# Optimization experiments

Hardware: AMD Instinct MI355X
Metric: run time of the kernel (lower is better)

Reference implementation:

```python
import jax, jax.numpy as jnp
import numpy as np

B, N, OUTERDIM, DIM, N_CLASSES = 2, 6000, 1024, 512, 2
HEADS, DIM_HEAD, INNER = 8, 64, 512
LANDMARKS, PINV_ITERS, KPAD = 256, 6, 16  # residual conv kernel 33 -> pad 16
SCALE = DIM_HEAD ** -0.5


def layer_norm(x, g, b, eps=1e-5):
    mu = x.mean(-1, keepdims=True)
    var = jnp.var(x, axis=-1, keepdims=True)
    return (x - mu) * jax.lax.rsqrt(var + eps) * g + b


def moore_penrose_pinv(x, iters=PINV_ITERS):
    # x: [b, h, m, m]
    abs_x = jnp.abs(x)
    col = abs_x.sum(-1)
    row = abs_x.sum(-2)
    z = jnp.swapaxes(x, -1, -2) / (jnp.max(col) * jnp.max(row))
    I = jnp.eye(x.shape[-1], dtype=x.dtype)
    for _ in range(iters):
        xz = x @ z
        z = 0.25 * z @ (13 * I - xz @ (15 * I - xz @ (7 * I - xz)))
    return z


def nystrom_attention(x, w_qkv, w_out, b_out, conv_w):
    b, n, _ = x.shape
    pad = (-n) % LANDMARKS
    xp = jnp.pad(x, ((0, 0), (pad, 0), (0, 0)))  # pad at FRONT, as in lucidrains impl
    npad = n + pad
    qkv = xp @ w_qkv.T  # [b, npad, 3*inner]
    q, k, v = [t.reshape(b, npad, HEADS, DIM_HEAD).transpose(0, 2, 1, 3)
               for t in jnp.split(qkv, 3, axis=-1)]
    q = q * SCALE
    l = npad // LANDMARKS  # tokens per landmark
    q_l = q.reshape(b, HEADS, LANDMARKS, l, DIM_HEAD).sum(3) / l
    k_l = k.reshape(b, HEADS, LANDMARKS, l, DIM_HEAD).sum(3) / l
    attn1 = jax.nn.softmax(jnp.einsum('bhid,bhjd->bhij', q, k_l), axis=-1)   # [b,h,npad,m]
    attn2 = jax.nn.softmax(jnp.einsum('bhid,bhjd->bhij', q_l, k_l), axis=-1)  # [b,h,m,m]
    attn3 = jax.nn.softmax(jnp.einsum('bhid,bhjd->bhij', q_l, k), axis=-1)    # [b,h,m,npad]
    out = (attn1 @ moore_penrose_pinv(attn2)) @ (attn3 @ v)  # [b,h,npad,d]
    # depthwise residual conv over sequence dim (per head), kernel (33,1)
    out = out + jax.lax.conv_general_dilated(
        v, conv_w, window_strides=(1, 1), padding=((KPAD, KPAD), (0, 0)),
        dimension_numbers=('NCHW', 'OIHW', 'NCHW'), feature_group_count=HEADS)
    out = out.transpose(0, 2, 1, 3).reshape(b, npad, INNER)
    out = out @ w_out.T + b_out
    return out[:, -n:]


def setup_inputs() -> dict:
    key = jax.random.key(0)
    ks = jax.random.split(key, 12)
    w = lambda k, shape: 0.02 * jax.random.normal(k, shape, dtype=jnp.float32)
    inp = {
        'data': jax.random.normal(ks[0], (B, N, OUTERDIM), dtype=jnp.float32),
        'w1': w(ks[1], (DIM, OUTERDIM)), 'b1': jnp.zeros((DIM,), jnp.float32),
        'cls_token': jax.random.normal(ks[2], (1, 1, DIM), dtype=jnp.float32),
        'ln1_g': jnp.ones((DIM,), jnp.float32), 'ln1_b': jnp.zeros((DIM,), jnp.float32),
        'qkv1_w': w(ks[3], (3 * INNER, DIM)),
        'out1_w': w(ks[4], (DIM, INNER)), 'out1_b': jnp.zeros((DIM,), jnp.float32),
        'conv1_w': w(ks[5], (HEADS, 1, 33, 1)),
        'ln2_g': jnp.ones((DIM,), jnp.float32), 'ln2_b': jnp.zeros((DIM,), jnp.float32),
        'qkv2_w': w(ks[6], (3 * INNER, DIM)),
        'out2_w': w(ks[7], (DIM, INNER)), 'out2_b': jnp.zeros((DIM,), jnp.float32),
        'conv2_w': w(ks[8], (HEADS, 1, 33, 1)),
        'lnf_g': jnp.ones((DIM,), jnp.float32), 'lnf_b': jnp.zeros((DIM,), jnp.float32),
        'w2': w(ks[9], (N_CLASSES, DIM)), 'b2': jnp.zeros((N_CLASSES,), jnp.float32),
    }
    return inp


def reference(data, w1, b1, cls_token, ln1_g, ln1_b, qkv1_w, out1_w, out1_b, conv1_w,
              ln2_g, ln2_b, qkv2_w, out2_w, out2_b, conv2_w, lnf_g, lnf_b, w2, b2):
    h = jax.nn.relu(data @ w1.T + b1)  # [B, N, DIM]
    H = h.shape[1]
    side = int(np.ceil(np.sqrt(H)))
    add = side * side - H
    h = jnp.concatenate([h, h[:, :add]], axis=1)  # square padding: 6084
    cls = jnp.broadcast_to(cls_token, (h.shape[0], 1, h.shape[2]))
    h = jnp.concatenate([cls, h], axis=1)  # +CLS: 6085
    h = h + nystrom_attention(layer_norm(h, ln1_g, ln1_b), qkv1_w, out1_w, out1_b, conv1_w)
    h = h + nystrom_attention(layer_norm(h, ln2_g, ln2_b), qkv2_w, out2_w, out2_b, conv2_w)
    h = layer_norm(h, lnf_g, lnf_b)[:, 0]
    logits = h @ w2.T + b2
    return logits
```

## Files before the change

### kernel.cpp

```cpp
#include <hip/hip_runtime.h>
#include <cstdint>
#include <cstddef>

namespace {

constexpr int DIMC  = 512;
constexpr int SEQ   = 6085;
constexpr int NPAD  = 6144;
constexpr int PADF  = 59;
constexpr int LMK   = 256;
constexpr int BHN   = 16;
constexpr int KSPL  = 16;
constexpr int MPADR = 6016;

typedef __attribute__((ext_vector_type(8))) short bf8_t;
typedef __attribute__((ext_vector_type(4))) float f4_t;

#define MFMA(a, b, c) __builtin_amdgcn_mfma_f32_16x16x32_bf16(a, b, c, 0, 0, 0)

#define SWZB(r, cu) (((((r) << 6) + ((cu) << 1))) ^ (((r) & 7) << 4))

#define GLDS16(gp, lp) __builtin_amdgcn_global_load_lds( \
    (const __attribute__((address_space(1))) void*)(gp), \
    (__attribute__((address_space(3))) void*)(lp), 16, 0, 0)

__device__ __forceinline__ ushort f2bf(float f) {
    union { float f; uint32_t u; } c{f};
    uint32_t u = c.u;
    return (ushort)((u + 0x7FFFu + ((u >> 16) & 1u)) >> 16);
}
__device__ __forceinline__ float bf2f(ushort u) {
    union { uint32_t u; float f; } c{(uint32_t)u << 16};
    return c.f;
}

__device__ __forceinline__ float waveSum(float v) {
#pragma unroll
    for (int o = 32; o > 0; o >>= 1) v += __shfl_xor(v, o, 64);
    return v;
}
__device__ __forceinline__ float waveMax(float v) {
#pragma unroll
    for (int o = 32; o > 0; o >>= 1) v = fmaxf(v, __shfl_xor(v, o, 64));
    return v;
}
__device__ __forceinline__ float blockSum256(float v, float* sm) {
    v = waveSum(v);
    __syncthreads();
    if ((threadIdx.x & 63) == 0) sm[threadIdx.x >> 6] = v;
    __syncthreads();
    return sm[0] + sm[1] + sm[2] + sm[3];
}
__device__ __forceinline__ float blockMax256(float v, float* sm) {
    v = waveMax(v);
    __syncthreads();
    if ((threadIdx.x & 63) == 0) sm[threadIdx.x >> 6] = v;
    __syncthreads();
    return fmaxf(fmaxf(sm[0], sm[1]), fmaxf(sm[2], sm[3]));
}
__device__ __forceinline__ float grpMax(float v) {
    v = fmaxf(v, __shfl_xor(v, 1, 64));
    v = fmaxf(v, __shfl_xor(v, 2, 64));
    v = fmaxf(v, __shfl_xor(v, 4, 64));
    v = fmaxf(v, __shfl_xor(v, 8, 64));
    return v;
}
__device__ __forceinline__ float grpSum(float v) {
    v += __shfl_xor(v, 1, 64);
    v += __shfl_xor(v, 2, 64);
    v += __shfl_xor(v, 4, 64);
    v += __shfl_xor(v, 8, 64);
    return v;
}

template<int EPI>
__global__ __launch_bounds__(256)
void gemm_bt(const ushort* __restrict__ A, const ushort* __restrict__ B,
             void* __restrict__ Cv, int M, int N, int K,
             int lda, int ldb, int ldc,
             long long sA, long long sB, long long sC,
             const float* __restrict__ bias, int relu,
             ushort* __restrict__ qp, ushort* __restrict__ kp, ushort* __restrict__ vp)
{
    __shared__ __align__(16) char As_s[128 * 128];
    __shared__ __align__(16) char Bs_s[128 * 128];
    const int z = blockIdx.z;
    const ushort* Ab = A + (size_t)z * sA;
    const ushort* Bb = B + (size_t)z * sB;
    const int row0 = blockIdx.y * 128, col0 = blockIdx.x * 128;
    const int tid = threadIdx.x, wid = tid >> 6, lane = tid & 63;
    const int wr = wid >> 1, wc = wid & 1, lr = lane & 15, kg = lane >> 4;
    const int srow = lane >> 3, sq = lane & 7;
    f4_t acc[4][4] = {};
    for (int k0 = 0; k0 < K; k0 += 64) {
        __syncthreads();
#pragma unroll
        for (int i = 0; i < 4; ++i) {
            int r = wid * 32 + i * 8 + srow;
            int qs = sq ^ (r & 7);
            GLDS16(Ab + (size_t)(row0 + r) * lda + k0 + qs * 8,
                   As_s + (wid * 32 + i * 8) * 128);
        }
#pragma unroll
        for (int i = 0; i < 4; ++i) {
            int r = wid * 32 + i * 8 + srow;
            int qs = sq ^ (r & 7);
            GLDS16(Bb + (size_t)(col0 + r) * ldb + k0 + qs * 8,
                   Bs_s + (wid * 32 + i * 8) * 128);
        }
        asm volatile("s_waitcnt vmcnt(0)" ::: "memory");
        __syncthreads();
#pragma unroll
        for (int ks = 0; ks < 2; ++ks) {
            bf8_t af[4], bg[4];
#pragma unroll
            for (int mr = 0; mr < 4; ++mr) {
                int r = wr * 64 + mr * 16 + lr;
                af[mr] = *(const bf8_t*)(As_s + r * 128 + ((((ks << 2) | kg) ^ (r & 7)) << 4));
            }
#pragma unroll
            for (int nr = 0; nr < 4; ++nr) {
                int r = wc * 64 + nr * 16 + lr;
                bg[nr] = *(const bf8_t*)(Bs_s + r * 128 + ((((ks << 2) | kg) ^ (r & 7)) << 4));
            }
#pragma unroll
            for (int mr = 0; mr < 4; ++mr)
#pragma unroll
                for (int nr = 0; nr < 4; ++nr)
                    acc[mr][nr] = MFMA(af[mr], bg[nr], acc[mr][nr]);
        }
    }
#pragma unroll
    for (int mr = 0; mr < 4; ++mr) {
#pragma unroll
        for (int nr = 0; nr < 4; ++nr) {
#pragma unroll
            for (int r = 0; r < 4; ++r) {
                int gm = row0 + wr * 64 + mr * 16 + kg * 4 + r;
                int gn = col0 + wc * 64 + nr * 16 + lr;
                if (gm >= M || gn >= N) continue;
                float val = acc[mr][nr][r];
                if (EPI == 0) {
                    if (bias) val += bias[gn];
                    if (relu) val = fmaxf(val, 0.f);
                    ((float*)Cv)[(size_t)z * sC + (size_t)gm * ldc + gn] = val;
                } else if (EPI == 1) {
                    ((ushort*)Cv)[(size_t)z * sC + (size_t)gm * ldc + gn] = f2bf(val);
                } else {
                    int b = (gm >= NPAD) ? 1 : 0;
                    int i = gm - b * NPAD;
                    int which = gn >> 9, hh = (gn >> 6) & 7, d = gn & 63;
                    if (which == 0)
                        qp[((size_t)(b * 8 + hh) * NPAD + i) * 64 + d] = f2bf(val * 0.125f);
                    else if (which == 1)
                        kp[((size_t)(b * 8 + hh) * NPAD + i) * 64 + d] = f2bf(val);
                    else
                        vp[((size_t)(b * 8 + hh) * 64 + d) * NPAD + i] = f2bf(val);
                }
            }
        }
    }
}

__global__ __launch_bounds__(256)
void pv_flash(const ushort* __restrict__ ql, const ushort* __restrict__ k,
              const ushort* __restrict__ vT, float* __restrict__ o2p,
              float* __restrict__ lmb, float* __restrict__ lsb)
{
    __shared__ __align__(16) char P_s[128 * 256];
    const int split = blockIdx.x, mt = blockIdx.y, bh = blockIdx.z;
    const int tid = threadIdx.x, wid = tid >> 6, lane = tid & 63;
    const int lr = lane & 15, kg = lane >> 4;
    const int rowb = wid * 32;
    const ushort* qlb = ql + ((size_t)bh * LMK + mt * 128) * 64;
    const ushort* kb  = k  + (size_t)bh * NPAD * 64;
    const ushort* vTb = vT + (size_t)bh * 64 * NPAD;
    const int kv0 = split * (NPAD / KSPL);

    float mrun[2][4], lrun[2][4];
    f4_t acco[2][4] = {};
#pragma unroll
    for (int mf = 0; mf < 2; ++mf)
#pragma unroll
        for (int r = 0; r < 4; ++r) { mrun[mf][r] = -3.0e38f; lrun[mf][r] = 0.f; }

    for (int kvt = 0; kvt < 3; ++kvt) {
        const int kvb = kv0 + kvt * 128;
        f4_t sacc[2][8] = {};
#pragma unroll
        for (int ks = 0; ks < 2; ++ks) {
            bf8_t af[2];
#pragma unroll
            for (int mf = 0; mf < 2; ++mf)
                af[mf] = *(const bf8_t*)&qlb[(size_t)(rowb + mf * 16 + lr) * 64 + ks * 32 + kg * 8];
#pragma unroll
            for (int nf = 0; nf < 8; ++nf) {
                bf8_t bg = *(const bf8_t*)&kb[(size_t)(kvb + nf * 16 + lr) * 64 + ks * 32 + kg * 8];
                sacc[0][nf] = MFMA(af[0], bg, sacc[0][nf]);
                sacc[1][nf] = MFMA(af[1], bg, sacc[1][nf]);
            }
        }
#pragma unroll
        for (int mf = 0; mf < 2; ++mf) {
            float tmax[4] = {-3.0e38f, -3.0e38f, -3.0e38f, -3.0e38f};
#pragma unroll
            for (int nf = 0; nf < 8; ++nf)
#pragma unroll
                for (int r = 0; r < 4; ++r) tmax[r] = fmaxf(tmax[r], sacc[mf][nf][r]);
#pragma unroll
            for (int r = 0; r < 4; ++r) {
                tmax[r] = grpMax(tmax[r]);
                float mnew = fmaxf(mrun[mf][r], tmax[r]);
                float sc = __expf(mrun[mf][r] - mnew);
                mrun[mf][r] = mnew;
                lrun[mf][r] *= sc;
#pragma unroll
                for (int nf2 = 0; nf2 < 4; ++nf2) acco[mf][nf2][r] *= sc;
            }
            float lsum[4] = {0.f, 0.f, 0.f, 0.f};
            const int rb2 = rowb + mf * 16 + kg * 4;
            const int cc2 = (lr & 7) * 2, chi = lr >> 3;
#pragma unroll
            for (int nf = 0; nf < 8; ++nf)
#pragma unroll
                for (int r = 0; r < 4; ++r) {
                    float e = __expf(sacc[mf][nf][r] - mrun[mf][r]);
                    lsum[r] += e;
                    int row = rb2 + r;
                    int chunk = (2 * nf + chi) ^ (row & 7);
                    *(ushort*)(P_s + row * 256 + chunk * 16 + cc2) = f2bf(e);
                }
#pragma unroll
            for (int r = 0; r < 4; ++r) lrun[mf][r] += grpSum(lsum[r]);
        }
#pragma unroll
        for (int kt2 = 0; kt2 < 4; ++kt2) {
            bf8_t af2[2];
#pragma unroll
            for (int mf = 0; mf < 2; ++mf) {
                int row = rowb + mf * 16 + lr;
                int chunk = (kt2 * 4 + kg) ^ (row & 7);
                af2[mf] = *(const bf8_t*)(P_s + row * 256 + chunk * 16);
            }
#pragma unroll
            for (int nf2 = 0; nf2 < 4; ++nf2) {
                bf8_t bg = *(const bf8_t*)&vTb[(size_t)(nf2 * 16 + lr) * NPAD + kvb + kt2 * 32 + kg * 8];
                acco[0][nf2] = MFMA(af2[0], bg, acco[0][nf2]);
                acco[1][nf2] = MFMA(af2[1], bg, acco[1][nf2]);
            }
        }
    }
#pragma unroll
    for (int mf = 0; mf < 2; ++mf)
#pragma unroll
        for (int nf2 = 0; nf2 < 4; ++nf2)
#pragma unroll
            for (int r = 0; r < 4; ++r) {
                int gm = mt * 128 + rowb + mf * 16 + kg * 4 + r;
                o2p[((size_t)(split * BHN + bh) * LMK + gm) * 64 + nf2 * 16 + lr] = acco[mf][nf2][r];
            }
    if (lr == 0) {
#pragma unroll
        for (int mf = 0; mf < 2; ++mf)
#pragma unroll
            for (int r = 0; r < 4; ++r) {
                int gm = mt * 128 + rowb + mf * 16 + kg * 4 + r;
                lmb[(size_t)(split * BHN + bh) * LMK + gm] = mrun[mf][r];
                lsb[(size_t)(split * BHN + bh) * LMK + gm] = lrun[mf][r];
            }
    }
}

__global__ void reduce_o2(const float* __restrict__ o2p, const float* __restrict__ lmb,
                          const float* __restrict__ lsb, ushort* __restrict__ o2)
{
    int idx = blockIdx.x * 256 + threadIdx.x;
    int bh = idx >> 14, m = (idx >> 6) & 255, d = idx & 63;
    float gm = -3.0e38f;
#pragma unroll
    for (int s = 0; s < KSPL; ++s)
        gm = fmaxf(gm, lmb[(size_t)(s * BHN + bh) * LMK + m]);
    float num = 0.f, den = 0.f;
#pragma unroll
    for (int s = 0; s < KSPL; ++s) {
        float wgt = __expf(lmb[(size_t)(s * BHN + bh) * LMK + m] - gm);
        num += wgt * o2p[((size_t)(s * BHN + bh) * LMK + m) * 64 + d];
        den += wgt * lsb[(size_t)(s * BHN + bh) * LMK + m];
    }
    o2[idx] = f2bf(num / den);
}

__global__ __launch_bounds__(256)
void attn1_fused(const ushort* __restrict__ q, const ushort* __restrict__ kl,
                 const ushort* __restrict__ Wt, ushort* __restrict__ ot)
{
    __shared__ __align__(16) char P_s[64 * 512];
    const int mt = blockIdx.x;
    const int bh = blockIdx.y;
    const int b = bh >> 3, hh = bh & 7;
    const int tid = threadIdx.x, wid = tid >> 6, lane = tid & 63;
    const int lr = lane & 15, kg = lane >> 4;
    const int row0 = mt * 64, rowb = wid * 16;
    const ushort* qb  = q  + (size_t)bh * NPAD * 64;
    const ushort* klb = kl + (size_t)bh * LMK * 64;
    const ushort* Wtb = Wt + (size_t)bh * 128 * 256;

    f4_t acc[16];
#pragma unroll
    for (int nf = 0; nf < 16; ++nf) acc[nf] = (f4_t){0.f, 0.f, 0.f, 0.f};
#pragma unroll
    for (int ks = 0; ks < 2; ++ks) {
        bf8_t af = *(const bf8_t*)&qb[(size_t)(row0 + rowb + lr) * 64 + ks * 32 + kg * 8];
#pragma unroll
        for (int nf = 0; nf < 16; ++nf) {
            bf8_t bg = *(const bf8_t*)&klb[(size_t)(nf * 16 + lr) * 64 + ks * 32 + kg * 8];
            acc[nf] = MFMA(af, bg, acc[nf]);
        }
    }
    float inv_s[4];
    {
        float mx[4] = {-3.0e38f, -3.0e38f, -3.0e38f, -3.0e38f};
#pragma unroll
        for (int nf = 0; nf < 16; ++nf)
#pragma unroll
            for (int r = 0; r < 4; ++r) mx[r] = fmaxf(mx[r], acc[nf][r]);
#pragma unroll
        for (int r = 0; r < 4; ++r) mx[r] = grpMax(mx[r]);
        float sum[4] = {0.f, 0.f, 0.f, 0.f};
        const int rb2 = rowb + kg * 4;
        const int cc2 = (lr & 7) * 2, chi = lr >> 3;
#pragma unroll
        for (int nf = 0; nf < 16; ++nf)
#pragma unroll
            for (int r = 0; r < 4; ++r) {
                float e = __expf(acc[nf][r] - mx[r]);
                sum[r] += e;
                int row = rb2 + r;
                int chunk = (2 * nf + chi) ^ (row & 7);
                *(ushort*)(P_s + row * 512 + chunk * 16 + cc2) = f2bf(e);
            }
#pragma unroll
        for (int r = 0; r < 4; ++r) inv_s[r] = 1.f / grpSum(sum[r]);
    }
    f4_t acc2[4] = {};
#pragma unroll
    for (int kt = 0; kt < 8; ++kt) {
        int row = rowb + lr;
        int chunk = (kt * 4 + kg) ^ (row & 7);
        bf8_t af2 = *(const bf8_t*)(P_s + row * 512 + chunk * 16);
#pragma unroll
        for (int nf = 0; nf < 4; ++nf) {
            bf8_t bg = *(const bf8_t*)&Wtb[(size_t)(nf * 16 + lr) * 256 + kt * 32 + kg * 8];
            acc2[nf] = MFMA(af2, bg, acc2[nf]);
        }
    }
#pragma unroll
    for (int nf = 0; nf < 4; ++nf)
#pragma unroll
        for (int r = 0; r < 4; ++r) {
            int gm = row0 + rowb + kg * 4 + r;
            int gn = nf * 16 + lr;
            ot[((size_t)(b * NPAD + gm)) * DIMC + hh * 64 + gn] = f2bf(acc2[nf][r] * inv_s[r]);
        }
}

__global__ __launch_bounds__(256)
void gemm_ns(const ushort* __restrict__ A, const ushort* __restrict__ B,
             ushort* __restrict__ C, ushort* __restrict__ C2, ushort* __restrict__ CT,
             float alpha, float c2d, int K, int N,
             long long sA, long long sB, long long sC, long long sCT)
{
    __shared__ __align__(16) char As_s[64 * 64];
    __shared__ __align__(16) char Bs_s[64 * 64];
    const int z = blockIdx.z;
    const int row0 = blockIdx.y * 64, col0 = blockIdx.x * 64;
    const int tid = threadIdx.x;
    const int wid = tid >> 6, lane = tid & 63;
    const int lr = lane & 15, kg = lane >> 4;
    const ushort* Ab = A + (size_t)z * sA;
    const ushort* Bb = B + (size_t)z * sB;
    f4_t acc[4] = {};
    const int am = tid >> 2, ac8 = (tid & 3) * 8;
    for (int k0 = 0; k0 < K; k0 += 32) {
        *(bf8_t*)(As_s + SWZB(am, ac8)) = *(const bf8_t*)&Ab[(size_t)(row0 + am) * K + k0 + ac8];
#pragma unroll
        for (int p = 0; p < 8; ++p) {
            int kk = p * 4 + (tid >> 6), n = tid & 63;
            *(ushort*)(Bs_s + SWZB(n, kk)) = Bb[(size_t)(k0 + kk) * N + col0 + n];
        }
        __syncthreads();
        bf8_t af = *(const bf8_t*)(As_s + SWZB(wid * 16 + lr, kg * 8));
#pragma unroll
        for (int j = 0; j < 4; ++j) {
            bf8_t bg = *(const bf8_t*)(Bs_s + SWZB(j * 16 + lr, kg * 8));
            acc[j] = MFMA(af, bg, acc[j]);
        }
        __syncthreads();
    }
#pragma unroll
    for (int j = 0; j < 4; ++j) {
#pragma unroll
        for (int r = 0; r < 4; ++r) {
            int gm = row0 + wid * 16 + kg * 4 + r;
            int gn = col0 + j * 16 + lr;
            float val = alpha * acc[j][r];
            if (C)  C[(size_t)z * sC + (size_t)gm * N + gn] = f2bf(val);
            if (C2) C2[(size_t)z * sC + (size_t)gm * N + gn] = f2bf(((gm == gn) ? c2d : 0.f) - val);
            if (CT) CT[(size_t)z * sCT + (size_t)gn * LMK + gm] = f2bf(val);
        }
    }
}

__global__ void cvt_bf16(const float* __restrict__ in, ushort* __restrict__ out, int n8) {
    int i = blockIdx.x * 256 + threadIdx.x;
    if (i >= n8) return;
    float4 a = ((const float4*)in)[i * 2], b = ((const float4*)in)[i * 2 + 1];
    ushort4 lo = { f2bf(a.x), f2bf(a.y), f2bf(a.z), f2bf(a.w) };
    ushort4 hi = { f2bf(b.x), f2bf(b.y), f2bf(b.z), f2bf(b.w) };
    ((ushort4*)out)[i * 2] = lo;
    ((ushort4*)out)[i * 2 + 1] = hi;
}

__global__ void extend_h(float* __restrict__ h, const float* __restrict__ cls) {
    int b = blockIdx.y, bx = blockIdx.x;
    float* hb = h + (size_t)b * SEQ * DIMC;
    for (int c = threadIdx.x; c < DIMC; c += 256) {
        if (bx == 0) hb[c] = cls[c];
        else hb[(size_t)(6000 + bx) * DIMC + c] = hb[(size_t)bx * DIMC + c];
    }
}

__global__ void zero_xp_pad(ushort* __restrict__ xp) {
    int e = blockIdx.x * 256 + threadIdx.x;
    int b = e / (PADF * DIMC);
    int rest = e - b * (PADF * DIMC);
    xp[(size_t)b * NPAD * DIMC + rest] = 0;
}

__global__ __launch_bounds__(128)
void ln_to_xp(const float* __restrict__ h, const float* __restrict__ g,
              const float* __restrict__ bb, ushort* __restrict__ xp)
{
    __shared__ float sm[2];
    int r = blockIdx.x;
    int b = r / SEQ, i = r - b * SEQ;
    int t = threadIdx.x;
    const float4* row = (const float4*)(h + (size_t)r * DIMC);
    float4 x = row[t];
    float s  = x.x + x.y + x.z + x.w;
    float sq = x.x * x.x + x.y * x.y + x.z * x.z + x.w * x.w;
    s = waveSum(s);
    sq = waveSum(sq);
    int w = t >> 6;
    if ((t & 63) == 0) sm[w] = s;
    __syncthreads();
    float S = sm[0] + sm[1];
    __syncthreads();
    if ((t & 63) == 0) sm[w] = sq;
    __syncthreads();
    float SQ = sm[0] + sm[1];
    float mu = S * (1.f / DIMC);
    float var = SQ * (1.f / DIMC) - mu * mu;
    float rs = rsqrtf(var + 1e-5f);
    float4 gg = ((const float4*)g)[t];
    float4 bv = ((const float4*)bb)[t];
    ushort4 o;
    o.x = f2bf((x.x - mu) * rs * gg.x + bv.x);
    o.y = f2bf((x.y - mu) * rs * gg.y + bv.y);
    o.z = f2bf((x.z - mu) * rs * gg.z + bv.z);
    o.w = f2bf((x.w - mu) * rs * gg.w + bv.w);
    ((ushort4*)(xp + ((size_t)b * NPAD + PADF + i) * DIMC))[t] = o;
}

__global__ void landmark_mean(const ushort* __restrict__ in, ushort* __restrict__ out) {
    int m = blockIdx.x, bh = blockIdx.y, d = threadIdx.x;
    const ushort* p = in + ((size_t)bh * NPAD + (size_t)m * (NPAD / LMK)) * 64 + d;
    float s = 0.f;
#pragma unroll
    for (int j = 0; j < NPAD / LMK; ++j) s += bf2f(p[(size_t)j * 64]);
    out[((size_t)bh * LMK + m) * 64 + d] = f2bf(s * (1.f / (NPAD / LMK)));
}

__global__ __launch_bounds__(256)
void softmax_bf256(ushort* __restrict__ S) {
    __shared__ float sm[4];
    ushort* p = S + (size_t)blockIdx.x * 256;
    int t = threadIdx.x;
    float v = bf2f(p[t]);
    float bm = blockMax256(v, sm);
    float e = __expf(v - bm);
    float bs = blockSum256(e, sm);
    p[t] = f2bf(e / bs);
}

__global__ __launch_bounds__(256)
void colsum_max(const ushort* __restrict__ X, float* __restrict__ scal) {
    __shared__ float sm[4];
    int bh = blockIdx.x, t = threadIdx.x;
    const ushort* Xb = X + ((size_t)bh << 16);
    float s = 0.f;
#pragma unroll 8
    for (int i = 0; i < 256; ++i) s += bf2f(Xb[(size_t)i * 256 + t]);
    float m = blockMax256(s, sm);
    if (t == 0) atomicMax((unsigned int*)scal, __float_as_uint(m));
}

__global__ void init_z(const ushort* __restrict__ X, const float* __restrict__ scal,
                       ushort* __restrict__ Z) {
    size_t e = (size_t)blockIdx.x * 256 + threadIdx.x;
    int c = (int)(e & 255);
    int r = (int)((e >> 8) & 255);
    size_t bh = e >> 16;
    float inv = 1.f / scal[0];
    Z[e] = f2bf(bf2f(X[(bh << 16) + (size_t)c * 256 + r]) * inv);
}

__global__ __launch_bounds__(256)
void conv_add(const ushort* __restrict__ vT, const float* __restrict__ cw,
              ushort* __restrict__ ot)
{
    __shared__ float w[33];
    __shared__ ushort vt[64][97];
    int bh = blockIdx.y;
    int b = bh >> 3, hh = bh & 7;
    int i0 = blockIdx.x * 64;
    int t = threadIdx.x;
    if (t < 33) w[t] = cw[hh * 33 + t];
    const ushort* vTb = vT + (size_t)bh * 64 * NPAD;
    for (int idx = t; idx < 64 * 96; idx += 256) {
        int d = idx / 96, jj = idx - d * 96;
        int j = i0 - 16 + jj;
        vt[d][jj] = (j >= 0 && j < NPAD) ? vTb[(size_t)d * NPAD + j] : (ushort)0;
    }
    __syncthreads();
    int d = t & 63;
    for (int ii = t >> 6; ii < 64; ii += 4) {
        float acc = 0.f;
#pragma unroll
        for (int kk = 0; kk < 33; ++kk) acc += w[kk] * bf2f(vt[d][ii + kk]);
        size_t off = ((size_t)(b * NPAD + i0 + ii)) * DIMC + hh * 64 + d;
        ot[off] = f2bf(bf2f(ot[off]) + acc);
    }
}

__global__ void residual_add(float* __restrict__ h, const float* __restrict__ y) {
    size_t e = (size_t)blockIdx.x * 256 + threadIdx.x;
    int c = (int)(e & 511);
    size_t ri = e >> 9;
    int i = (int)(ri % SEQ);
    int b = (int)(ri / SEQ);
    h[e] += y[((size_t)b * NPAD + PADF + i) * DIMC + c];
}

__global__ __launch_bounds__(256)
void final_head(const float* __restrict__ h, const float* __restrict__ g,
                const float* __restrict__ bb, const float* __restrict__ w2,
                const float* __restrict__ b2, float* __restrict__ out)
{
    __shared__ float row[DIMC];
    __shared__ float sm[4];
    int b = blockIdx.x;
    int t = threadIdx.x;
    const float* x = h + (size_t)b * SEQ * DIMC;
    float v0 = x[t], v1 = x[t + 256];
    float S = blockSum256(v0 + v1, sm);
    float SQ = blockSum256(v0 * v0 + v1 * v1, sm);
    float mu = S * (1.f / DIMC);
    float rs = rsqrtf(SQ * (1.f / DIMC) - mu * mu + 1e-5f);
    row[t] = (v0 - mu) * rs * g[t] + bb[t];
    row[t + 256] = (v1 - mu) * rs * g[t + 256] + bb[t + 256];
    __syncthreads();
    if (t < 64) {
        float a0 = 0.f, a1 = 0.f;
        for (int idx = t; idx < DIMC; idx += 64) {
            a0 += row[idx] * w2[idx];
            a1 += row[idx] * w2[DIMC + idx];
        }
        a0 = waveSum(a0);
        a1 = waveSum(a1);
        if (t == 0) {
            out[b * 2 + 0] = a0 + b2[0];
            out[b * 2 + 1] = a1 + b2[1];
        }
    }
}

void bt(int epi, const ushort* A, const ushort* B, void* C, int M, int N, int K,
        int lda, int ldb, int ldc, long long sA, long long sB, long long sC, int batch,
        const float* bias, int relu, ushort* qp, ushort* kp, ushort* vp, hipStream_t s)
{
    dim3 g((N + 127) / 128, (M + 127) / 128, batch), blk(256);
    switch (epi) {
    case 0: gemm_bt<0><<<g, blk, 0, s>>>(A, B, C, M, N, K, lda, ldb, ldc, sA, sB, sC, bias, relu, qp, kp, vp); break;
    case 1: gemm_bt<1><<<g, blk, 0, s>>>(A, B, C, M, N, K, lda, ldb, ldc, sA, sB, sC, bias, relu, qp, kp, vp); break;
    default: gemm_bt<2><<<g, blk, 0, s>>>(A, B, C, M, N, K, lda, ldb, ldc, sA, sB, sC, bias, relu, qp, kp, vp); break;
    }
}

void ns(const ushort* A, const ushort* B, ushort* C, ushort* C2, ushort* CT,
        float alpha, float c2d, int M, int N, int K,
        long long sA, long long sB, long long sC, long long sCT, hipStream_t s)
{
    dim3 g(N / 64, M / 64, BHN), blk(256);
    gemm_ns<<<g, blk, 0, s>>>(A, B, C, C2, CT, alpha, c2d, K, N, sA, sB, sC, sCT);
}

struct WS {
    float *h, *scal, *o2p, *y, *lmb, *lsb;
    ushort *xp, *q, *k, *vT, *ql, *kl;
    ushort *datab, *w1b, *qkvwb1, *qkvwb2, *outwb1, *outwb2;
    ushort *X, *Z0, *Z1, *XZ, *TA, *TB, *TC;
    ushort *o2b, *Wt, *S, *ot;
};

void nystrom_layer(float* h, const float* lng, const float* lnb,
                   const ushort* qkvwb, const ushort* outwb, const float* outb,
                   const float* convw, const WS& w, hipStream_t s)
{
    const long long SM = (long long)LMK * LMK;
    zero_xp_pad<<<(2 * PADF * DIMC) / 256, 256, 0, s>>>(w.xp);
    ln_to_xp<<<2 * SEQ, 128, 0, s>>>(h, lng, lnb, w.xp);
    bt(2, w.xp, qkvwb, nullptr, 2 * NPAD, 3 * DIMC, DIMC, DIMC, DIMC, 0,
       0, 0, 0, 1, nullptr, 0, w.q, w.k, w.vT, s);
    landmark_mean<<<dim3(LMK, BHN), 64, 0, s>>>(w.q, w.ql);
    landmark_mean<<<dim3(LMK, BHN), 64, 0, s>>>(w.k, w.kl);
    bt(1, w.ql, w.kl, w.X, LMK, LMK, 64, 64, 64, LMK,
       (long long)LMK * 64, (long long)LMK * 64, SM, BHN, nullptr, 0, nullptr, nullptr, nullptr, s);
    softmax_bf256<<<BHN * LMK, 256, 0, s>>>(w.X);
    hipMemsetAsync(w.scal, 0, 8, s);
    colsum_max<<<BHN, 256, 0, s>>>(w.X, w.scal);
    init_z<<<(BHN * LMK * LMK) / 256, 256, 0, s>>>(w.X, w.scal, w.Z0);
    ushort* Zc = w.Z0;
    ushort* Zn = w.Z1;
    for (int it = 0; it < 6; ++it) {
        ns(w.X, Zc, w.XZ, w.TA, nullptr, 1.f, 7.f, LMK, LMK, LMK, SM, SM, SM, 0, s);
        ns(w.XZ, w.TA, w.TB, w.TC, nullptr, 1.f, 15.f, LMK, LMK, LMK, SM, SM, SM, 0, s);
        ns(w.XZ, w.TC, w.TB, w.TA, nullptr, 1.f, 13.f, LMK, LMK, LMK, SM, SM, SM, 0, s);
        ns(Zc, w.TA, Zn, nullptr, nullptr, 0.25f, 0.f, LMK, LMK, LMK, SM, SM, SM, 0, s);
        ushort* t = Zc; Zc = Zn; Zn = t;
    }
    pv_flash<<<dim3(KSPL, 2, BHN), 256, 0, s>>>(w.ql, w.k, w.vT, w.o2p, w.lmb, w.lsb);
    reduce_o2<<<BHN * LMK * 64 / 256, 256, 0, s>>>(w.o2p, w.lmb, w.lsb, w.o2b);
    ns(Zc, w.o2b, nullptr, nullptr, w.Wt, 1.f, 0.f, LMK, 64, LMK,
       SM, (long long)LMK * 64, 0, 128 * 256, s);
    attn1_fused<<<dim3(NPAD / 64, BHN), 256, 0, s>>>(w.q, w.kl, w.Wt, w.ot);
    conv_add<<<dim3(NPAD / 64, BHN), 256, 0, s>>>(w.vT, convw, w.ot);
    bt(0, w.ot, outwb, w.y, 2 * NPAD, DIMC, DIMC, DIMC, DIMC, DIMC,
       0, 0, 0, 1, outb, 0, nullptr, nullptr, nullptr, s);
    residual_add<<<(2 * SEQ * DIMC) / 256, 256, 0, s>>>(h, w.y);
}

}

extern "C" void kernel_launch(void* const* d_in, const int* in_sizes, int n_in,
                              void* d_out, int out_size, void* d_ws, size_t ws_size,
                              hipStream_t stream)
{
    (void)in_sizes; (void)n_in; (void)out_size;
    const float* data  = (const float*)d_in[0];
    const float* w1    = (const float*)d_in[1];
    const float* b1    = (const float*)d_in[2];
    const float* cls   = (const float*)d_in[3];
    const float* ln1g  = (const float*)d_in[4];
    const float* ln1b  = (const float*)d_in[5];
    const float* qkv1w = (const float*)d_in[6];
    const float* out1w = (const float*)d_in[7];
    const float* out1b = (const float*)d_in[8];
    const float* conv1 = (const float*)d_in[9];
    const float* ln2g  = (const float*)d_in[10];
    const float* ln2b  = (const float*)d_in[11];
    const float* qkv2w = (const float*)d_in[12];
    const float* out2w = (const float*)d_in[13];
    const float* out2b = (const float*)d_in[14];
    const float* conv2 = (const float*)d_in[15];
    const float* lnfg  = (const float*)d_in[16];
    const float* lnfb  = (const float*)d_in[17];
    const float* w2    = (const float*)d_in[18];
    const float* b2    = (const float*)d_in[19];
    float* out = (float*)d_out;

    if (ws_size < 209473792ull) return;
    char* p = (char*)d_ws;
    auto alloc = [&](size_t bytes) { char* r = p; p += (bytes + 255) & ~(size_t)255; return r; };
    WS w;
    w.h     = (float*)alloc((size_t)2 * SEQ * DIMC * 4);
    w.xp    = (ushort*)alloc((size_t)2 * NPAD * DIMC * 2);
    w.q     = (ushort*)alloc((size_t)BHN * NPAD * 64 * 2);
    w.k     = (ushort*)alloc((size_t)BHN * NPAD * 64 * 2);
    w.vT    = (ushort*)alloc((size_t)BHN * 64 * NPAD * 2);
    w.ql    = (ushort*)alloc((size_t)BHN * LMK * 64 * 2);
    w.kl    = (ushort*)alloc((size_t)BHN * LMK * 64 * 2);
    w.scal  = (float*)alloc(256);
    w.datab = (ushort*)alloc((size_t)2 * MPADR * 1024 * 2);
    w.w1b   = (ushort*)alloc((size_t)512 * 1024 * 2);
    w.qkvwb1= (ushort*)alloc((size_t)1536 * 512 * 2);
    w.qkvwb2= (ushort*)alloc((size_t)1536 * 512 * 2);
    w.outwb1= (ushort*)alloc((size_t)512 * 512 * 2);
    w.outwb2= (ushort*)alloc((size_t)512 * 512 * 2);
    w.X     = (ushort*)alloc((size_t)BHN * LMK * LMK * 2);
    w.Z0    = (ushort*)alloc((size_t)BHN * LMK * LMK * 2);
    w.Z1    = (ushort*)alloc((size_t)BHN * LMK * LMK * 2);
    w.XZ    = (ushort*)alloc((size_t)BHN * LMK * LMK * 2);
    w.TA    = (ushort*)alloc((size_t)BHN * LMK * LMK * 2);
    w.TB    = (ushort*)alloc((size_t)BHN * LMK * LMK * 2);
    w.TC    = (ushort*)alloc((size_t)BHN * LMK * LMK * 2);
    w.o2p   = (float*)alloc((size_t)KSPL * BHN * LMK * 64 * 4);
    w.lmb   = (float*)alloc((size_t)KSPL * BHN * LMK * 4);
    w.lsb   = (float*)alloc((size_t)KSPL * BHN * LMK * 4);
    w.o2b   = (ushort*)alloc((size_t)BHN * LMK * 64 * 2);
    w.Wt    = (ushort*)alloc((size_t)BHN * 128 * 256 * 2);
    w.S     = (ushort*)alloc((size_t)BHN * LMK * NPAD * 2);
    w.y     = (float*)w.S;
    w.ot    = w.k;

    for (int b = 0; b < 2; ++b)
        cvt_bf16<<<3000, 256, 0, stream>>>(data + (size_t)b * 6000 * 1024,
                                           w.datab + (size_t)b * MPADR * 1024, 768000);
    cvt_bf16<<<256, 256, 0, stream>>>(w1, w.w1b, 65536);
    cvt_bf16<<<384, 256, 0, stream>>>(qkv1w, w.qkvwb1, 98304);
    cvt_bf16<<<384, 256, 0, stream>>>(qkv2w, w.qkvwb2, 98304);
    cvt_bf16<<<128, 256, 0, stream>>>(out1w, w.outwb1, 32768);
    cvt_bf16<<<128, 256, 0, stream>>>(out2w, w.outwb2, 32768);

    bt(0, w.datab, w.w1b, w.h + DIMC, 6000, DIMC, 1024, 1024, 1024, DIMC,
       (long long)MPADR * 1024, 0, (long long)SEQ * DIMC, 2, b1, 1,
       nullptr, nullptr, nullptr, stream);
    extend_h<<<dim3(85, 2), 256, 0, stream>>>(w.h, cls);

    nystrom_layer(w.h, ln1g, ln1b, w.qkvwb1, w.outwb1, out1b, conv1, w, stream);
    nystrom_layer(w.h, ln2g, ln2b, w.qkvwb2, w.outwb2, out2b, conv2, w, stream);

    final_head<<<2, 256, 0, stream>>>(w.h, lnfg, lnfb, w2, b2, out);
}
```

Before: 1.094 ms.

## Replace flash-style attn3 with materialized softmax and direct-load NS GEMMs

Replaces the LDS-tiled Newton-Schulz GEMM with a direct-from-global MFMA kernel. It keeps transposed copies of the iterate matrices so both operands are read along K, and uses the polynomial matrices' symmetry (they are all polynomials in the same XZ product) to emit transposed outputs. The online-softmax attn3 kernel is replaced by three steps: materialize the full ql·kᵀ score matrix, run a row softmax over it, then do a plain split-K P·V product. This removes the running max/sum bookkeeping and the rescale reduction. In exchange it writes and re-reads a large bf16 score buffer in global memory and adds launches.

```diff
diff --git a/kernel.cpp b/kernel.cpp
--- a/kernel.cpp
+++ b/kernel.cpp
@@ -17,8 +17,6 @@
 typedef __attribute__((ext_vector_type(4))) float f4_t;
 
 #define MFMA(a, b, c) __builtin_amdgcn_mfma_f32_16x16x32_bf16(a, b, c, 0, 0, 0)
-
-#define SWZB(r, cu) (((((r) << 6) + ((cu) << 1))) ^ (((r) & 7) << 4))
 
 #define GLDS16(gp, lp) __builtin_amdgcn_global_load_lds( \
     (const __attribute__((address_space(1))) void*)(gp), \
@@ -162,132 +160,87 @@
     }
 }
 
-__global__ __launch_bounds__(256)
-void pv_flash(const ushort* __restrict__ ql, const ushort* __restrict__ k,
-              const ushort* __restrict__ vT, float* __restrict__ o2p,
-              float* __restrict__ lmb, float* __restrict__ lsb)
-{
-    __shared__ __align__(16) char P_s[128 * 256];
+template<int OC, int OCT, int CTD>
+__global__ __launch_bounds__(256)
+void gemm_d(const ushort* __restrict__ A, const ushort* __restrict__ Bt,
+            ushort* __restrict__ C, ushort* __restrict__ CT,
+            float alpha, float cd, int K, int ldC, int ldCT,
+            long long sA, long long sBt, long long sC, long long sCT)
+{
+    const int z = blockIdx.z;
+    const int row0 = blockIdx.y * 64, col0 = blockIdx.x * 64;
+    const int tid = threadIdx.x, wid = tid >> 6, lane = tid & 63;
+    const int lr = lane & 15, kg = lane >> 4;
+    const ushort* Ab = A + (size_t)z * sA + (size_t)(row0 + wid * 16 + lr) * K;
+    const ushort* Bb = Bt + (size_t)z * sBt + (size_t)(col0 + lr) * K;
+    f4_t acc[4] = {};
+#pragma unroll 2
+    for (int k0 = 0; k0 < K; k0 += 32) {
+        bf8_t af = *(const bf8_t*)&Ab[k0 + kg * 8];
+#pragma unroll
+        for (int nf = 0; nf < 4; ++nf) {
+            bf8_t bg = *(const bf8_t*)&Bb[(size_t)nf * 16 * K + k0 + kg * 8];
+            acc[nf] = MFMA(af, bg, acc[nf]);
+        }
+    }
+#pragma unroll
+    for (int nf = 0; nf < 4; ++nf) {
+#pragma unroll
+        for (int r = 0; r < 4; ++r) {
+            int gm = row0 + wid * 16 + kg * 4 + r;
+            int gn = col0 + nf * 16 + lr;
+            float val = alpha * acc[nf][r];
+            if (OC) C[(size_t)z * sC + (size_t)gm * ldC + gn] = f2bf(val);
+            if (OCT) CT[(size_t)z * sCT + (size_t)gn * ldCT + gm] =
+                f2bf(CTD ? (((gm == gn) ? cd : 0.f) - val) : val);
+        }
+    }
+}
+
+__global__ __launch_bounds__(256)
+void pv_direct(const ushort* __restrict__ S, const ushort* __restrict__ vT,
+               float* __restrict__ o2p)
+{
     const int split = blockIdx.x, mt = blockIdx.y, bh = blockIdx.z;
     const int tid = threadIdx.x, wid = tid >> 6, lane = tid & 63;
     const int lr = lane & 15, kg = lane >> 4;
-    const int rowb = wid * 32;
-    const ushort* qlb = ql + ((size_t)bh * LMK + mt * 128) * 64;
-    const ushort* kb  = k  + (size_t)bh * NPAD * 64;
+    const ushort* Sb = S + (size_t)bh * LMK * NPAD;
     const ushort* vTb = vT + (size_t)bh * 64 * NPAD;
-    const int kv0 = split * (NPAD / KSPL);
-
-    float mrun[2][4], lrun[2][4];
-    f4_t acco[2][4] = {};
+    const int ks0 = split * (NPAD / KSPL);
+    f4_t acc[2][4] = {};
+#pragma unroll 2
+    for (int k0 = ks0; k0 < ks0 + NPAD / KSPL; k0 += 32) {
+        bf8_t af[2];
+#pragma unroll
+        for (int mf = 0; mf < 2; ++mf)
+            af[mf] = *(const bf8_t*)&Sb[(size_t)(mt * 128 + wid * 32 + mf * 16 + lr) * NPAD + k0 + kg * 8];
+#pragma unroll
+        for (int nf = 0; nf < 4; ++nf) {
+            bf8_t bg = *(const bf8_t*)&vTb[(size_t)(nf * 16 + lr) * NPAD + k0 + kg * 8];
+            acc[0][nf] = MFMA(af[0], bg, acc[0][nf]);
+            acc[1][nf] = MFMA(af[1], bg, acc[1][nf]);
+        }
+    }
 #pragma unroll
     for (int mf = 0; mf < 2; ++mf)
 #pragma unroll
-        for (int r = 0; r < 4; ++r) { mrun[mf][r] = -3.0e38f; lrun[mf][r] = 0.f; }
-
-    for (int kvt = 0; kvt < 3; ++kvt) {
-        const int kvb = kv0 + kvt * 128;
-        f4_t sacc[2][8] = {};
-#pragma unroll
-        for (int ks = 0; ks < 2; ++ks) {
-            bf8_t af[2];
-#pragma unroll
-            for (int mf = 0; mf < 2; ++mf)
-                af[mf] = *(const bf8_t*)&qlb[(size_t)(rowb + mf * 16 + lr) * 64 + ks * 32 + kg * 8];
-#pragma unroll
-            for (int nf = 0; nf < 8; ++nf) {
-                bf8_t bg = *(const bf8_t*)&kb[(size_t)(kvb + nf * 16 + lr) * 64 + ks * 32 + kg * 8];
-                sacc[0][nf] = MFMA(af[0], bg, sacc[0][nf]);
-                sacc[1][nf] = MFMA(af[1], bg, sacc[1][nf]);
+        for (int nf = 0; nf < 4; ++nf)
+#pragma unroll
+            for (int r = 0; r < 4; ++r) {
+                int gm = mt * 128 + wid * 32 + mf * 16 + kg * 4 + r;
+                int gn = nf * 16 + lr;
+                o2p[((size_t)(split * BHN + bh) * LMK + gm) * 64 + gn] = acc[mf][nf][r];
             }
-        }
-#pragma unroll
-        for (int mf = 0; mf < 2; ++mf) {
-            float tmax[4] = {-3.0e38f, -3.0e38f, -3.0e38f, -3.0e38f};
-#pragma unroll
-            for (int nf = 0; nf < 8; ++nf)
-#pragma unroll
-                for (int r = 0; r < 4; ++r) tmax[r] = fmaxf(tmax[r], sacc[mf][nf][r]);
-#pragma unroll
-            for (int r = 0; r < 4; ++r) {
-                tmax[r] = grpMax(tmax[r]);
-                float mnew = fmaxf(mrun[mf][r], tmax[r]);
-                float sc = __expf(mrun[mf][r] - mnew);
-                mrun[mf][r] = mnew;
-                lrun[mf][r] *= sc;
-#pragma unroll
-                for (int nf2 = 0; nf2 < 4; ++nf2) acco[mf][nf2][r] *= sc;
-            }
-            float lsum[4] = {0.f, 0.f, 0.f, 0.f};
-            const int rb2 = rowb + mf * 16 + kg * 4;
-            const int cc2 = (lr & 7) * 2, chi = lr >> 3;
-#pragma unroll
-            for (int nf = 0; nf < 8; ++nf)
-#pragma unroll
-                for (int r = 0; r < 4; ++r) {
-                    float e = __expf(sacc[mf][nf][r] - mrun[mf][r]);
-                    lsum[r] += e;
-                    int row = rb2 + r;
-                    int chunk = (2 * nf + chi) ^ (row & 7);
-                    *(ushort*)(P_s + row * 256 + chunk * 16 + cc2) = f2bf(e);
-                }
-#pragma unroll
-            for (int r = 0; r < 4; ++r) lrun[mf][r] += grpSum(lsum[r]);
-        }
-#pragma unroll
-        for (int kt2 = 0; kt2 < 4; ++kt2) {
-            bf8_t af2[2];
-#pragma unroll
-            for (int mf = 0; mf < 2; ++mf) {
-                int row = rowb + mf * 16 + lr;
-                int chunk = (kt2 * 4 + kg) ^ (row & 7);
-                af2[mf] = *(const bf8_t*)(P_s + row * 256 + chunk * 16);
-            }
-#pragma unroll
-            for (int nf2 = 0; nf2 < 4; ++nf2) {
-                bf8_t bg = *(const bf8_t*)&vTb[(size_t)(nf2 * 16 + lr) * NPAD + kvb + kt2 * 32 + kg * 8];
-                acco[0][nf2] = MFMA(af2[0], bg, acco[0][nf2]);
-                acco[1][nf2] = MFMA(af2[1], bg, acco[1][nf2]);
-            }
-        }
-    }
-#pragma unroll
-    for (int mf = 0; mf < 2; ++mf)
-#pragma unroll
-        for (int nf2 = 0; nf2 < 4; ++nf2)
-#pragma unroll
-            for (int r = 0; r < 4; ++r) {
-                int gm = mt * 128 + rowb + mf * 16 + kg * 4 + r;
-                o2p[((size_t)(split * BHN + bh) * LMK + gm) * 64 + nf2 * 16 + lr] = acco[mf][nf2][r];
-            }
-    if (lr == 0) {
-#pragma unroll
-        for (int mf = 0; mf < 2; ++mf)
-#pragma unroll
-            for (int r = 0; r < 4; ++r) {
-                int gm = mt * 128 + rowb + mf * 16 + kg * 4 + r;
-                lmb[(size_t)(split * BHN + bh) * LMK + gm] = mrun[mf][r];
-                lsb[(size_t)(split * BHN + bh) * LMK + gm] = lrun[mf][r];
-            }
-    }
-}
-
-__global__ void reduce_o2(const float* __restrict__ o2p, const float* __restrict__ lmb,
-                          const float* __restrict__ lsb, ushort* __restrict__ o2)
-{
+}
+
+__global__ void reduce_o2(const float* __restrict__ o2p, ushort* __restrict__ o2t) {
     int idx = blockIdx.x * 256 + threadIdx.x;
     int bh = idx >> 14, m = (idx >> 6) & 255, d = idx & 63;
-    float gm = -3.0e38f;
-#pragma unroll
-    for (int s = 0; s < KSPL; ++s)
-        gm = fmaxf(gm, lmb[(size_t)(s * BHN + bh) * LMK + m]);
-    float num = 0.f, den = 0.f;
-#pragma unroll
-    for (int s = 0; s < KSPL; ++s) {
-        float wgt = __expf(lmb[(size_t)(s * BHN + bh) * LMK + m] - gm);
-        num += wgt * o2p[((size_t)(s * BHN + bh) * LMK + m) * 64 + d];
-        den += wgt * lsb[(size_t)(s * BHN + bh) * LMK + m];
-    }
-    o2[idx] = f2bf(num / den);
+    float s = 0.f;
+#pragma unroll
+    for (int sp = 0; sp < KSPL; ++sp)
+        s += o2p[((size_t)(sp * BHN + bh) << 14) + (m << 6) + d];
+    o2t[((size_t)bh * 64 + d) * 256 + m] = f2bf(s);
 }
 
 __global__ __launch_bounds__(256)
@@ -362,53 +315,6 @@
             int gn = nf * 16 + lr;
             ot[((size_t)(b * NPAD + gm)) * DIMC + hh * 64 + gn] = f2bf(acc2[nf][r] * inv_s[r]);
         }
-}
-
-__global__ __launch_bounds__(256)
-void gemm_ns(const ushort* __restrict__ A, const ushort* __restrict__ B,
-             ushort* __restrict__ C, ushort* __restrict__ C2, ushort* __restrict__ CT,
-             float alpha, float c2d, int K, int N,
-             long long sA, long long sB, long long sC, long long sCT)
-{
-    __shared__ __align__(16) char As_s[64 * 64];
-    __shared__ __align__(16) char Bs_s[64 * 64];
-    const int z = blockIdx.z;
-    const int row0 = blockIdx.y * 64, col0 = blockIdx.x * 64;
-    const int tid = threadIdx.x;
-    const int wid = tid >> 6, lane = tid & 63;
-    const int lr = lane & 15, kg = lane >> 4;
-    const ushort* Ab = A + (size_t)z * sA;
-    const ushort* Bb = B + (size_t)z * sB;
-    f4_t acc[4] = {};
-    const int am = tid >> 2, ac8 = (tid & 3) * 8;
-    for (int k0 = 0; k0 < K; k0 += 32) {
-        *(bf8_t*)(As_s + SWZB(am, ac8)) = *(const bf8_t*)&Ab[(size_t)(row0 + am) * K + k0 + ac8];
-#pragma unroll
-        for (int p = 0; p < 8; ++p) {
-            int kk = p * 4 + (tid >> 6), n = tid & 63;
-            *(ushort*)(Bs_s + SWZB(n, kk)) = Bb[(size_t)(k0 + kk) * N + col0 + n];
-        }
-        __syncthreads();
-        bf8_t af = *(const bf8_t*)(As_s + SWZB(wid * 16 + lr, kg * 8));
-#pragma unroll
-        for (int j = 0; j < 4; ++j) {
-            bf8_t bg = *(const bf8_t*)(Bs_s + SWZB(j * 16 + lr, kg * 8));
-            acc[j] = MFMA(af, bg, acc[j]);
-        }
-        __syncthreads();
-    }
-#pragma unroll
-    for (int j = 0; j < 4; ++j) {
-#pragma unroll
-        for (int r = 0; r < 4; ++r) {
-            int gm = row0 + wid * 16 + kg * 4 + r;
-            int gn = col0 + j * 16 + lr;
-            float val = alpha * acc[j][r];
-            if (C)  C[(size_t)z * sC + (size_t)gm * N + gn] = f2bf(val);
-            if (C2) C2[(size_t)z * sC + (size_t)gm * N + gn] = f2bf(((gm == gn) ? c2d : 0.f) - val);
-            if (CT) CT[(size_t)z * sCT + (size_t)gn * LMK + gm] = f2bf(val);
-        }
-    }
 }
 
 __global__ void cvt_bf16(const float* __restrict__ in, ushort* __restrict__ out, int n8) {
@@ -482,6 +388,25 @@
 }
 
 __global__ __launch_bounds__(256)
+void softmax_bf_wide(ushort* __restrict__ S) {
+    __shared__ float sm[4];
+    ushort* p = S + (size_t)blockIdx.x * NPAD;
+    int t = threadIdx.x;
+    float v[24];
+    float mx = -1e30f;
+#pragma unroll
+    for (int j = 0; j < 24; ++j) { v[j] = bf2f(p[j * 256 + t]); mx = fmaxf(mx, v[j]); }
+    float bm = blockMax256(mx, sm);
+    float s = 0.f;
+#pragma unroll
+    for (int j = 0; j < 24; ++j) { v[j] = __expf(v[j] - bm); s += v[j]; }
+    float bs = blockSum256(s, sm);
+    float inv = 1.f / bs;
+#pragma unroll
+    for (int j = 0; j < 24; ++j) p[j * 256 + t] = f2bf(v[j] * inv);
+}
+
+__global__ __launch_bounds__(256)
 void softmax_bf256(ushort* __restrict__ S) {
     __shared__ float sm[4];
     ushort* p = S + (size_t)blockIdx.x * 256;
@@ -506,13 +431,14 @@
 }
 
 __global__ void init_z(const ushort* __restrict__ X, const float* __restrict__ scal,
-                       ushort* __restrict__ Z) {
+                       ushort* __restrict__ Z, ushort* __restrict__ Zt) {
     size_t e = (size_t)blockIdx.x * 256 + threadIdx.x;
     int c = (int)(e & 255);
     int r = (int)((e >> 8) & 255);
     size_t bh = e >> 16;
     float inv = 1.f / scal[0];
-    Z[e] = f2bf(bf2f(X[(bh << 16) + (size_t)c * 256 + r]) * inv);
+    Z[e]  = f2bf(bf2f(X[(bh << 16) + (size_t)c * 256 + r]) * inv);
+    Zt[e] = f2bf(bf2f(X[e]) * inv);
 }
 
 __global__ __launch_bounds__(256)
@@ -597,20 +523,12 @@
     }
 }
 
-void ns(const ushort* A, const ushort* B, ushort* C, ushort* C2, ushort* CT,
-        float alpha, float c2d, int M, int N, int K,
-        long long sA, long long sB, long long sC, long long sCT, hipStream_t s)
-{
-    dim3 g(N / 64, M / 64, BHN), blk(256);
-    gemm_ns<<<g, blk, 0, s>>>(A, B, C, C2, CT, alpha, c2d, K, N, sA, sB, sC, sCT);
-}
-
 struct WS {
-    float *h, *scal, *o2p, *y, *lmb, *lsb;
+    float *h, *scal, *o2p, *y;
     ushort *xp, *q, *k, *vT, *ql, *kl;
     ushort *datab, *w1b, *qkvwb1, *qkvwb2, *outwb1, *outwb2;
-    ushort *X, *Z0, *Z1, *XZ, *TA, *TB, *TC;
-    ushort *o2b, *Wt, *S, *ot;
+    ushort *X, *Y, *TA, *TB, *Z0, *Z0t, *Z1, *Z1t;
+    ushort *o2t, *Wt, *S, *ot;
 };
 
 void nystrom_layer(float* h, const float* lng, const float* lnb,
@@ -618,31 +536,42 @@
                    const float* convw, const WS& w, hipStream_t s)
 {
     const long long SM = (long long)LMK * LMK;
+    const long long S64 = (long long)LMK * 64;
+    dim3 blk(256);
     zero_xp_pad<<<(2 * PADF * DIMC) / 256, 256, 0, s>>>(w.xp);
     ln_to_xp<<<2 * SEQ, 128, 0, s>>>(h, lng, lnb, w.xp);
     bt(2, w.xp, qkvwb, nullptr, 2 * NPAD, 3 * DIMC, DIMC, DIMC, DIMC, 0,
        0, 0, 0, 1, nullptr, 0, w.q, w.k, w.vT, s);
     landmark_mean<<<dim3(LMK, BHN), 64, 0, s>>>(w.q, w.ql);
     landmark_mean<<<dim3(LMK, BHN), 64, 0, s>>>(w.k, w.kl);
-    bt(1, w.ql, w.kl, w.X, LMK, LMK, 64, 64, 64, LMK,
-       (long long)LMK * 64, (long long)LMK * 64, SM, BHN, nullptr, 0, nullptr, nullptr, nullptr, s);
+    gemm_d<1, 0, 0><<<dim3(4, 4, BHN), blk, 0, s>>>(w.ql, w.kl, w.X, nullptr,
+        1.f, 0.f, 64, 256, 0, S64, S64, SM, 0);
     softmax_bf256<<<BHN * LMK, 256, 0, s>>>(w.X);
     hipMemsetAsync(w.scal, 0, 8, s);
     colsum_max<<<BHN, 256, 0, s>>>(w.X, w.scal);
-    init_z<<<(BHN * LMK * LMK) / 256, 256, 0, s>>>(w.X, w.scal, w.Z0);
-    ushort* Zc = w.Z0;
-    ushort* Zn = w.Z1;
+    init_z<<<(BHN * LMK * LMK) / 256, 256, 0, s>>>(w.X, w.scal, w.Z0, w.Z0t);
+    ushort *Zc = w.Z0, *Zct = w.Z0t, *Zn = w.Z1, *Znt = w.Z1t;
+    dim3 gns(4, 4, BHN);
     for (int it = 0; it < 6; ++it) {
-        ns(w.X, Zc, w.XZ, w.TA, nullptr, 1.f, 7.f, LMK, LMK, LMK, SM, SM, SM, 0, s);
-        ns(w.XZ, w.TA, w.TB, w.TC, nullptr, 1.f, 15.f, LMK, LMK, LMK, SM, SM, SM, 0, s);
-        ns(w.XZ, w.TC, w.TB, w.TA, nullptr, 1.f, 13.f, LMK, LMK, LMK, SM, SM, SM, 0, s);
-        ns(Zc, w.TA, Zn, nullptr, nullptr, 0.25f, 0.f, LMK, LMK, LMK, SM, SM, SM, 0, s);
-        ushort* t = Zc; Zc = Zn; Zn = t;
-    }
-    pv_flash<<<dim3(KSPL, 2, BHN), 256, 0, s>>>(w.ql, w.k, w.vT, w.o2p, w.lmb, w.lsb);
-    reduce_o2<<<BHN * LMK * 64 / 256, 256, 0, s>>>(w.o2p, w.lmb, w.lsb, w.o2b);
-    ns(Zc, w.o2b, nullptr, nullptr, w.Wt, 1.f, 0.f, LMK, 64, LMK,
-       SM, (long long)LMK * 64, 0, 128 * 256, s);
+        gemm_d<1, 1, 1><<<gns, blk, 0, s>>>(w.X, Zct, w.Y, w.TA,
+            1.f, 7.f, 256, 256, 256, SM, SM, SM, SM);
+        gemm_d<0, 1, 1><<<gns, blk, 0, s>>>(w.Y, w.TA, nullptr, w.TB,
+            1.f, 15.f, 256, 0, 256, SM, SM, 0, SM);
+        gemm_d<0, 1, 1><<<gns, blk, 0, s>>>(w.Y, w.TB, nullptr, w.TA,
+            1.f, 13.f, 256, 0, 256, SM, SM, 0, SM);
+        gemm_d<1, 1, 0><<<gns, blk, 0, s>>>(Zc, w.TA, Zn, Znt,
+            0.25f, 0.f, 256, 256, 256, SM, SM, SM, SM);
+        ushort* t;
+        t = Zc; Zc = Zn; Zn = t;
+        t = Zct; Zct = Znt; Znt = t;
+    }
+    gemm_d<1, 0, 0><<<dim3(NPAD / 64, 4, BHN), blk, 0, s>>>(w.ql, w.k, w.S, nullptr,
+        1.f, 0.f, 64, NPAD, 0, S64, (long long)NPAD * 64, (long long)LMK * NPAD, 0);
+    softmax_bf_wide<<<BHN * LMK, 256, 0, s>>>(w.S);
+    pv_direct<<<dim3(KSPL, 2, BHN), 256, 0, s>>>(w.S, w.vT, w.o2p);
+    reduce_o2<<<BHN * LMK * 64 / 256, 256, 0, s>>>(w.o2p, w.o2t);
+    gemm_d<0, 1, 0><<<dim3(1, 4, BHN), blk, 0, s>>>(Zc, w.o2t, nullptr, w.Wt,
+        1.f, 0.f, 256, 0, 256, SM, 64 * 256, 0, 128 * 256);
     attn1_fused<<<dim3(NPAD / 64, BHN), 256, 0, s>>>(w.q, w.kl, w.Wt, w.ot);
     conv_add<<<dim3(NPAD / 64, BHN), 256, 0, s>>>(w.vT, convw, w.ot);
     bt(0, w.ot, outwb, w.y, 2 * NPAD, DIMC, DIMC, DIMC, DIMC, DIMC,
@@ -698,16 +627,15 @@
     w.outwb1= (ushort*)alloc((size_t)512 * 512 * 2);
     w.outwb2= (ushort*)alloc((size_t)512 * 512 * 2);
     w.X     = (ushort*)alloc((size_t)BHN * LMK * LMK * 2);
-    w.Z0    = (ushort*)alloc((size_t)BHN * LMK * LMK * 2);
-    w.Z1    = (ushort*)alloc((size_t)BHN * LMK * LMK * 2);
-    w.XZ    = (ushort*)alloc((size_t)BHN * LMK * LMK * 2);
+    w.Y     = (ushort*)alloc((size_t)BHN * LMK * LMK * 2);
     w.TA    = (ushort*)alloc((size_t)BHN * LMK * LMK * 2);
     w.TB    = (ushort*)alloc((size_t)BHN * LMK * LMK * 2);
-    w.TC    = (ushort*)alloc((size_t)BHN * LMK * LMK * 2);
+    w.Z0    = (ushort*)alloc((size_t)BHN * LMK * LMK * 2);
+    w.Z0t   = (ushort*)alloc((size_t)BHN * LMK * LMK * 2);
+    w.Z1    = (ushort*)alloc((size_t)BHN * LMK * LMK * 2);
+    w.Z1t   = (ushort*)alloc((size_t)BHN * LMK * LMK * 2);
     w.o2p   = (float*)alloc((size_t)KSPL * BHN * LMK * 64 * 4);
-    w.lmb   = (float*)alloc((size_t)KSPL * BHN * LMK * 4);
-    w.lsb   = (float*)alloc((size_t)KSPL * BHN * LMK * 4);
-    w.o2b   = (ushort*)alloc((size_t)BHN * LMK * 64 * 2);
+    w.o2t   = (ushort*)alloc((size_t)BHN * 64 * 256 * 2);
     w.Wt    = (ushort*)alloc((size_t)BHN * 128 * 256 * 2);
     w.S     = (ushort*)alloc((size_t)BHN * LMK * NPAD * 2);
     w.y     = (float*)w.S;
```

Measured after the change: 1.195 ms. 9.2% more time.
